# Kernel tuning notes

Hardware: AMD Instinct MI355X
Metric: run time of the kernel (lower is better)

The kernel has to match this reference:

```python
import jax, jax.numpy as jnp
import numpy as np

N_EMB = 256
HEAD_SIZE = 64
B, S = 4, 4096


def setup_inputs() -> dict:
    key = jax.random.key(0)
    k1, k2, k3, k4 = jax.random.split(key, 4)
    return {
        "ini_emb": jax.random.normal(k1, (B, S, N_EMB), dtype=jnp.float32),
        "wk": jax.random.normal(k2, (N_EMB, HEAD_SIZE), dtype=jnp.float32) * (N_EMB ** -0.5),
        "wq": jax.random.normal(k3, (N_EMB, HEAD_SIZE), dtype=jnp.float32) * (N_EMB ** -0.5),
        "wv": jax.random.normal(k4, (N_EMB, HEAD_SIZE), dtype=jnp.float32) * (N_EMB ** -0.5),
    }


def reference(ini_emb, wk, wq, wv):
    # projections: [B,S,E] @ [E,H] -> [B,S,H]
    k = ini_emb @ wk
    q = ini_emb @ wq
    v = ini_emb @ wv
    # scores: [B,S,S]; NOTE: source scales by n_emb**-0.5, not head_size**-0.5
    scores = jnp.einsum("bqh,bkh->bqk", q, k) * (N_EMB ** -0.5)
    attn = jax.nn.softmax(scores, axis=-1)
    # output: [B,S,H]
    return jnp.einsum("bqk,bkh->bqh", attn, v)
```

## Files before the change

kernel.cpp:

```cpp
#include <hip/hip_runtime.h>


typedef short short4v __attribute__((ext_vector_type(4)));
typedef short short8v __attribute__((ext_vector_type(8)));
typedef float floatx4 __attribute__((ext_vector_type(4)));
typedef unsigned short u16;
typedef unsigned int u32;

#define SEQ 4096
#define EMB 256
#define HD 64
#define PADA 264
#define OSTR 68

static __device__ __forceinline__ u16 f2bf(float x) {
    union { float f; unsigned u; } v; v.f = x;
    unsigned r = v.u + 0x7FFFu + ((v.u >> 16) & 1u);
    return (u16)(r >> 16);
}

static __device__ __forceinline__ u32 cvt_pk_bf16(float a, float b) {
    u32 r;
    asm("v_cvt_pk_bf16_f32 %0, %1, %2" : "=v"(r) : "v"(a), "v"(b));
    return r;
}

static __device__ __forceinline__ short4v pack_bf4(float a, float b, float c, float d) {
    union { u32 u[2]; short4v s; } x;
    x.u[0] = cvt_pk_bf16(a, b);
    x.u[1] = cvt_pk_bf16(c, d);
    return x.s;
}

__global__ __launch_bounds__(256) void prep_w(
    const float* __restrict__ wk, const float* __restrict__ wq, const float* __restrict__ wv,
    u16* __restrict__ wt) {
    const int nt = blockIdx.x;
    const int t = threadIdx.x;
#pragma unroll
    for (int ss = 0; ss < 2; ++ss) {
        int slot = t + ss * 256;
        int kc = slot >> 6, lane = slot & 63;
        int ln15 = lane & 15, lq = lane >> 4;
        int cg = nt * 16 + ln15;
        int mat = cg >> 6, col = cg & 63;
        const float* W = (mat == 0) ? wq : (mat == 1) ? wk : wv;
        const float s = (mat == 0) ? 0.0625f * 1.44269504088896f : 1.0f;
        u32 w4[4];
#pragma unroll
        for (int p = 0; p < 2; ++p) {
#pragma unroll
            for (int d = 0; d < 2; ++d) {
                int e0 = kc * 32 + lq * 8 + p * 4 + d * 2;
                u16 lo = f2bf(W[(e0 + 0) * HD + col] * s);
                u16 hi = f2bf(W[(e0 + 1) * HD + col] * s);
                w4[p * 2 + d] = (u32)lo | ((u32)hi << 16);
            }
        }
        u32* dst = (u32*)wt + ((size_t)(nt * 8 + kc) * 64 + lane) * 4;
        *(uint4*)dst = make_uint4(w4[0], w4[1], w4[2], w4[3]);
    }
}

__global__ __launch_bounds__(256) void proj_mfma(
    const float* __restrict__ emb, const u16* __restrict__ wt,
    u16* __restrict__ qb, u16* __restrict__ kb, u16* __restrict__ vbt) {
    __shared__ u16 a_s[16 * PADA];
    const int t = threadIdx.x;
    const int lane = t & 63;
    const int wave = t >> 6;
    const int ln15 = lane & 15;
    const int lq = lane >> 4;
    const size_t row0 = (size_t)blockIdx.x * 16;

#pragma unroll
    for (int c = 0; c < 4; ++c) {
        int f = t + c * 256;
        int row = f >> 6, e4 = (f & 63) * 4;
        float4 v = *(const float4*)(emb + (row0 + row) * EMB + e4);
        u32 lo = cvt_pk_bf16(v.x, v.y);
        u32 hi = cvt_pk_bf16(v.z, v.w);
        *(uint2*)&a_s[row * PADA + e4] = make_uint2(lo, hi);
    }
    __syncthreads();

    floatx4 acc[3];
#pragma unroll
    for (int j = 0; j < 3; ++j) {
        floatx4 z = { 0.f, 0.f, 0.f, 0.f };
        acc[j] = z;
    }

#pragma unroll
    for (int kc = 0; kc < 8; ++kc) {
        short8v a = *(const short8v*)&a_s[ln15 * PADA + kc * 32 + lq * 8];
#pragma unroll
        for (int j = 0; j < 3; ++j) {
            short8v b = *(const short8v*)(wt + (((size_t)(wave * 3 + j) * 8 + kc) * 64 + lane) * 8);
            acc[j] = __builtin_amdgcn_mfma_f32_16x16x32_bf16(a, b, acc[j], 0, 0, 0);
        }
    }

#pragma unroll
    for (int j = 0; j < 3; ++j) {
        int cg = (wave * 3 + j) * 16 + ln15;
        int mat = cg >> 6, col = cg & 63;
        if (mat < 2) {
            u16* O = (mat == 0) ? qb : kb;
#pragma unroll
            for (int r = 0; r < 4; ++r)
                O[(row0 + lq * 4 + r) * HD + col] = f2bf(acc[j][r]);
        } else {
            u32 lo = cvt_pk_bf16(acc[j][0], acc[j][1]);
            u32 hi = cvt_pk_bf16(acc[j][2], acc[j][3]);
            size_t bidx = row0 >> 12;
            size_t sl = (row0 & 4095) + lq * 4;
            *(uint2*)&vbt[(bidx * 64 + col) * SEQ + sl] = make_uint2(lo, hi);
        }
    }
}


__global__ __launch_bounds__(256) void attn_kernel(
    const u16* __restrict__ qb, const u16* __restrict__ kb, const u16* __restrict__ vbt,
    float* __restrict__ po, float* __restrict__ pml) {
    __shared__ __align__(16) u16 smem[4][64 * 64];
    __shared__ float lred[4 * 64];

    const int t = threadIdx.x;
    const int lane = t & 63;
    const int wave = t >> 6;
    const int ln15 = lane & 15;
    const int lq = lane >> 4;

    const int part = ((blockIdx.x & 7) << 6) | (blockIdx.x >> 3);
    const int b = part >> 7;
    const int qt = (part >> 1) & 63;
    const int split = part & 1;
    const int q0 = qt * 64;

    const u16* __restrict__ qpb = qb + ((size_t)b * SEQ + q0) * HD;
    const u16* __restrict__ kpb = kb + (size_t)b * SEQ * HD;
    const u16* __restrict__ vpb = vbt + (size_t)b * HD * SEQ;

    short8v qf[4][2];
#pragma unroll
    for (int nt = 0; nt < 4; ++nt)
#pragma unroll
        for (int h = 0; h < 2; ++h)
            qf[nt][h] = *(const short8v*)(qpb + (size_t)(nt * 16 + ln15) * HD + h * 32 + lq * 8);

    floatx4 oacc[4][4];
#pragma unroll
    for (int ht = 0; ht < 4; ++ht)
#pragma unroll
        for (int nt = 0; nt < 4; ++nt) {
            floatx4 z = { 0.f, 0.f, 0.f, 0.f };
            oacc[ht][nt] = z;
        }
    float lacc[4] = { 0.f, 0.f, 0.f, 0.f };

    const int r0 = t >> 3, c0 = t & 7;
    const int r1 = (t + 256) >> 3, c1 = t & 7;
    const int sw0 = r0 * 64 + ((c0 ^ (r0 & 7)) * 8);
    const int sw1 = r1 * 64 + ((c1 ^ (r1 & 7)) * 8);

    const int krow = wave * 16 + ln15;
    const int ksw_lo = krow * 64 + (((0 + lq) ^ (ln15 & 7)) * 8);
    const int ksw_hi = krow * 64 + (((4 + lq) ^ (ln15 & 7)) * 8);
    const int vch = wave * 2 + (lq >> 1);
    const int voff = ((vch ^ (ln15 & 7)) * 8) + (lq & 1) * 4;

    uint4 ka, kb4, va, vb4;
    {
        const int kwb = (split * 32) * 64;
        ka  = *(const uint4*)(kpb + (size_t)(kwb + r0) * HD + c0 * 8);
        kb4 = *(const uint4*)(kpb + (size_t)(kwb + r1) * HD + c1 * 8);
        va  = *(const uint4*)(vpb + (size_t)r0 * SEQ + kwb + c0 * 8);
        vb4 = *(const uint4*)(vpb + (size_t)r1 * SEQ + kwb + c1 * 8);
        *(uint4*)(&smem[0][0] + sw0) = ka;
        *(uint4*)(&smem[0][0] + sw1) = kb4;
        *(uint4*)(&smem[1][0] + sw0) = va;
        *(uint4*)(&smem[1][0] + sw1) = vb4;
    }
    __syncthreads();

#pragma unroll 1
    for (int tt = 0; tt < 32; ++tt) {
        const int buf = tt & 1;
        if (tt < 31) {
            const int kwb = (split * 32 + tt + 1) * 64;
            ka  = *(const uint4*)(kpb + (size_t)(kwb + r0) * HD + c0 * 8);
            kb4 = *(const uint4*)(kpb + (size_t)(kwb + r1) * HD + c1 * 8);
            va  = *(const uint4*)(vpb + (size_t)r0 * SEQ + kwb + c0 * 8);
            vb4 = *(const uint4*)(vpb + (size_t)r1 * SEQ + kwb + c1 * 8);
        }

        const u16* kt = &smem[buf * 2 + 0][0];
        const u16* vt = &smem[buf * 2 + 1][0];

        short4v vf[4];
#pragma unroll
        for (int ht = 0; ht < 4; ++ht)
            vf[ht] = *(const short4v*)(vt + (ht * 16 + ln15) * 64 + voff);

        short8v k0 = *(const short8v*)(kt + ksw_lo);
        short8v k1 = *(const short8v*)(kt + ksw_hi);

        floatx4 s[4];
        __builtin_amdgcn_s_setprio(1);
#pragma unroll
        for (int nt = 0; nt < 4; ++nt) {
            floatx4 z = { 0.f, 0.f, 0.f, 0.f };
            s[nt] = __builtin_amdgcn_mfma_f32_16x16x32_bf16(k0, qf[nt][0], z, 0, 0, 0);
            s[nt] = __builtin_amdgcn_mfma_f32_16x16x32_bf16(k1, qf[nt][1], s[nt], 0, 0, 0);
        }
        __builtin_amdgcn_s_setprio(0);

        short4v pf[4];
#pragma unroll
        for (int nt = 0; nt < 4; ++nt) {
            float p0 = __builtin_amdgcn_exp2f(s[nt][0]);
            float p1 = __builtin_amdgcn_exp2f(s[nt][1]);
            float p2 = __builtin_amdgcn_exp2f(s[nt][2]);
            float p3 = __builtin_amdgcn_exp2f(s[nt][3]);
            lacc[nt] += (p0 + p1) + (p2 + p3);
            pf[nt] = pack_bf4(p0, p1, p2, p3);
        }

        __builtin_amdgcn_s_setprio(1);
#pragma unroll
        for (int ht = 0; ht < 4; ++ht)
#pragma unroll
            for (int nt = 0; nt < 4; ++nt)
                oacc[ht][nt] = __builtin_amdgcn_mfma_f32_16x16x16bf16_1k(
                    vf[ht], pf[nt], oacc[ht][nt], 0, 0, 0);
        __builtin_amdgcn_s_setprio(0);

        if (tt < 31) {
            u16* ktn = &smem[(buf ^ 1) * 2 + 0][0];
            u16* vtn = &smem[(buf ^ 1) * 2 + 1][0];
            *(uint4*)(ktn + sw0) = ka;
            *(uint4*)(ktn + sw1) = kb4;
            *(uint4*)(vtn + sw0) = va;
            *(uint4*)(vtn + sw1) = vb4;
        }
        __syncthreads();
    }

#pragma unroll
    for (int nt = 0; nt < 4; ++nt) {
        lacc[nt] += __shfl_xor(lacc[nt], 16);
        lacc[nt] += __shfl_xor(lacc[nt], 32);
    }
    if (lq == 0) {
#pragma unroll
        for (int nt = 0; nt < 4; ++nt)
            lred[wave * 64 + nt * 16 + ln15] = lacc[nt];
    }

    float* ored = (float*)&smem[0][0];
    for (int s4 = 0; s4 < 4; ++s4) {
        if (wave == s4) {
#pragma unroll
            for (int nt = 0; nt < 4; ++nt)
#pragma unroll
                for (int ht = 0; ht < 4; ++ht) {
                    int idx = (nt * 16 + ln15) * OSTR + ht * 16 + lq * 4;
                    if (s4 == 0) {
                        *(floatx4*)&ored[idx] = oacc[ht][nt];
                    } else {
                        floatx4 old = *(floatx4*)&ored[idx];
                        old += oacc[ht][nt];
                        *(floatx4*)&ored[idx] = old;
                    }
                }
        }
        __syncthreads();
    }

    float* __restrict__ pob = po + (size_t)part * 4096;
#pragma unroll
    for (int i = 0; i < 4; ++i) {
        int f4 = t + i * 256;
        int q = f4 >> 4, h4 = (f4 & 15) * 4;
        *(float4*)&pob[q * HD + h4] = *(float4*)&ored[q * OSTR + h4];
    }
    if (t < 64)
        pml[part * 64 + t] = lred[t] + lred[64 + t] + lred[128 + t] + lred[192 + t];
}

__global__ __launch_bounds__(256) void reduce_kernel(
    const float* __restrict__ po, const float* __restrict__ pml,
    float* __restrict__ out) {
    __shared__ float ls[64];
    const int t = threadIdx.x;
    const int part0 = blockIdx.x * 2;
    const int bq = blockIdx.x;

    if (t < 64)
        ls[t] = pml[(part0 + 0) * 64 + t] + pml[(part0 + 1) * 64 + t];
    __syncthreads();

    const float* __restrict__ p0 = po + (size_t)(part0 + 0) * 4096;
    const float* __restrict__ p1 = po + (size_t)(part0 + 1) * 4096;
    float* __restrict__ ob = out + (((size_t)(bq >> 6) * SEQ + (size_t)(bq & 63) * 64)) * HD;

#pragma unroll
    for (int i = 0; i < 4; ++i) {
        int f4 = t + i * 256;
        int f = f4 * 4;
        int q = f4 >> 4;
        float4 a = *(const float4*)&p0[f];
        float4 c = *(const float4*)&p1[f];
        float inv = 1.0f / ls[q];
        float4 r;
        r.x = (a.x + c.x) * inv;
        r.y = (a.y + c.y) * inv;
        r.z = (a.z + c.z) * inv;
        r.w = (a.w + c.w) * inv;
        *(float4*)&ob[f] = r;
    }
}

extern "C" void kernel_launch(void* const* d_in, const int* in_sizes, int n_in,
                              void* d_out, int out_size, void* d_ws, size_t ws_size,
                              hipStream_t stream) {
    const float* emb = (const float*)d_in[0];
    const float* wk  = (const float*)d_in[1];
    const float* wq  = (const float*)d_in[2];
    const float* wv  = (const float*)d_in[3];

    u16* qb  = (u16*)d_ws;
    u16* kb  = (u16*)((char*)d_ws + (size_t)2 * 1024 * 1024);
    u16* vbt = (u16*)((char*)d_ws + (size_t)4 * 1024 * 1024);
    u16* wt  = (u16*)((char*)d_ws + (size_t)6 * 1024 * 1024);
    float* po  = (float*)((char*)d_ws + (size_t)6 * 1024 * 1024 + 256 * 1024);
    float* pml = (float*)((char*)d_ws + (size_t)22 * 1024 * 1024 + 256 * 1024);
    float* out = (float*)d_out;

    prep_w<<<12, 256, 0, stream>>>(wk, wq, wv, wt);
    proj_mfma<<<1024, 256, 0, stream>>>(emb, wt, qb, kb, vbt);
    attn_kernel<<<512, 256, 0, stream>>>(qb, kb, vbt, po, pml);
    reduce_kernel<<<256, 256, 0, stream>>>(po, pml, out);
}
```

Baseline: 112.7 us.

## Partition queries across waves with 128-query blocks and four-way KV split

The attention kernel now gives each block 128 queries and a quarter of the keys instead of 64 queries and half the keys. Each wave owns 32 query rows and loops over all 64 keys of the tile, where before each wave took 16 keys for all 64 queries. This removes the cross-wave LDS reduction of the output accumulators and the partial sums, so each wave writes its partials straight to global memory. The cost is more global partial data (four splits of 8192 floats per block), a reduce kernel that sums four partials, and more LDS reads per wave for K and V fragments.

```diff
diff --git a/kernel.cpp b/kernel.cpp
--- a/kernel.cpp
+++ b/kernel.cpp
@@ -11,7 +11,6 @@
 #define EMB 256
 #define HD 64
 #define PADA 264
-#define OSTR 68
 
 static __device__ __forceinline__ u16 f2bf(float x) {
     union { float f; unsigned u; } v; v.f = x;
@@ -125,7 +124,6 @@
     const u16* __restrict__ qb, const u16* __restrict__ kb, const u16* __restrict__ vbt,
     float* __restrict__ po, float* __restrict__ pml) {
     __shared__ __align__(16) u16 smem[4][64 * 64];
-    __shared__ float lred[4 * 64];
 
     const int t = threadIdx.x;
     const int lane = t & 63;
@@ -135,49 +133,47 @@
 
     const int part = ((blockIdx.x & 7) << 6) | (blockIdx.x >> 3);
     const int b = part >> 7;
-    const int qt = (part >> 1) & 63;
-    const int split = part & 1;
-    const int q0 = qt * 64;
+    const int qblk = (part >> 2) & 31;
+    const int split = part & 3;
+    const int q0 = qblk * 128;
 
     const u16* __restrict__ qpb = qb + ((size_t)b * SEQ + q0) * HD;
     const u16* __restrict__ kpb = kb + (size_t)b * SEQ * HD;
     const u16* __restrict__ vpb = vbt + (size_t)b * HD * SEQ;
 
-    short8v qf[4][2];
-#pragma unroll
-    for (int nt = 0; nt < 4; ++nt)
+    short8v qf[2][2];
+#pragma unroll
+    for (int nt = 0; nt < 2; ++nt)
 #pragma unroll
         for (int h = 0; h < 2; ++h)
-            qf[nt][h] = *(const short8v*)(qpb + (size_t)(nt * 16 + ln15) * HD + h * 32 + lq * 8);
-
-    floatx4 oacc[4][4];
+            qf[nt][h] = *(const short8v*)(qpb + (size_t)(wave * 32 + nt * 16 + ln15) * HD + h * 32 + lq * 8);
+
+    floatx4 oacc[4][2];
 #pragma unroll
     for (int ht = 0; ht < 4; ++ht)
 #pragma unroll
-        for (int nt = 0; nt < 4; ++nt) {
+        for (int nt = 0; nt < 2; ++nt) {
             floatx4 z = { 0.f, 0.f, 0.f, 0.f };
             oacc[ht][nt] = z;
         }
-    float lacc[4] = { 0.f, 0.f, 0.f, 0.f };
-
-    const int r0 = t >> 3, c0 = t & 7;
-    const int r1 = (t + 256) >> 3, c1 = t & 7;
+    float lacc[2] = { 0.f, 0.f };
+
+    const int r0 = t >> 3, c0 = t & 7, r1 = r0 + 32;
     const int sw0 = r0 * 64 + ((c0 ^ (r0 & 7)) * 8);
-    const int sw1 = r1 * 64 + ((c1 ^ (r1 & 7)) * 8);
-
-    const int krow = wave * 16 + ln15;
-    const int ksw_lo = krow * 64 + (((0 + lq) ^ (ln15 & 7)) * 8);
-    const int ksw_hi = krow * 64 + (((4 + lq) ^ (ln15 & 7)) * 8);
-    const int vch = wave * 2 + (lq >> 1);
-    const int voff = ((vch ^ (ln15 & 7)) * 8) + (lq & 1) * 4;
+    const int sw1 = r1 * 64 + ((c0 ^ (r1 & 7)) * 8);
+
+    const int xk = ln15 & 7;
+    const int ksw_lo = ln15 * 64 + ((lq ^ xk) * 8);
+    const int ksw_hi = ln15 * 64 + (((4 + lq) ^ xk) * 8);
+    const int vch0 = lq >> 1, vsub = (lq & 1) * 4;
 
     uint4 ka, kb4, va, vb4;
     {
-        const int kwb = (split * 32) * 64;
+        const int kwb = (split * 16) * 64;
         ka  = *(const uint4*)(kpb + (size_t)(kwb + r0) * HD + c0 * 8);
-        kb4 = *(const uint4*)(kpb + (size_t)(kwb + r1) * HD + c1 * 8);
+        kb4 = *(const uint4*)(kpb + (size_t)(kwb + r1) * HD + c0 * 8);
         va  = *(const uint4*)(vpb + (size_t)r0 * SEQ + kwb + c0 * 8);
-        vb4 = *(const uint4*)(vpb + (size_t)r1 * SEQ + kwb + c1 * 8);
+        vb4 = *(const uint4*)(vpb + (size_t)r1 * SEQ + kwb + c0 * 8);
         *(uint4*)(&smem[0][0] + sw0) = ka;
         *(uint4*)(&smem[0][0] + sw1) = kb4;
         *(uint4*)(&smem[1][0] + sw0) = va;
@@ -186,58 +182,59 @@
     __syncthreads();
 
 #pragma unroll 1
-    for (int tt = 0; tt < 32; ++tt) {
+    for (int tt = 0; tt < 16; ++tt) {
         const int buf = tt & 1;
-        if (tt < 31) {
-            const int kwb = (split * 32 + tt + 1) * 64;
+        if (tt < 15) {
+            const int kwb = (split * 16 + tt + 1) * 64;
             ka  = *(const uint4*)(kpb + (size_t)(kwb + r0) * HD + c0 * 8);
-            kb4 = *(const uint4*)(kpb + (size_t)(kwb + r1) * HD + c1 * 8);
+            kb4 = *(const uint4*)(kpb + (size_t)(kwb + r1) * HD + c0 * 8);
             va  = *(const uint4*)(vpb + (size_t)r0 * SEQ + kwb + c0 * 8);
-            vb4 = *(const uint4*)(vpb + (size_t)r1 * SEQ + kwb + c1 * 8);
-        }
-
-        const u16* kt = &smem[buf * 2 + 0][0];
-        const u16* vt = &smem[buf * 2 + 1][0];
-
-        short4v vf[4];
-#pragma unroll
-        for (int ht = 0; ht < 4; ++ht)
-            vf[ht] = *(const short4v*)(vt + (ht * 16 + ln15) * 64 + voff);
-
-        short8v k0 = *(const short8v*)(kt + ksw_lo);
-        short8v k1 = *(const short8v*)(kt + ksw_hi);
-
-        floatx4 s[4];
-        __builtin_amdgcn_s_setprio(1);
-#pragma unroll
-        for (int nt = 0; nt < 4; ++nt) {
-            floatx4 z = { 0.f, 0.f, 0.f, 0.f };
-            s[nt] = __builtin_amdgcn_mfma_f32_16x16x32_bf16(k0, qf[nt][0], z, 0, 0, 0);
-            s[nt] = __builtin_amdgcn_mfma_f32_16x16x32_bf16(k1, qf[nt][1], s[nt], 0, 0, 0);
-        }
-        __builtin_amdgcn_s_setprio(0);
-
-        short4v pf[4];
-#pragma unroll
-        for (int nt = 0; nt < 4; ++nt) {
-            float p0 = __builtin_amdgcn_exp2f(s[nt][0]);
-            float p1 = __builtin_amdgcn_exp2f(s[nt][1]);
-            float p2 = __builtin_amdgcn_exp2f(s[nt][2]);
-            float p3 = __builtin_amdgcn_exp2f(s[nt][3]);
-            lacc[nt] += (p0 + p1) + (p2 + p3);
-            pf[nt] = pack_bf4(p0, p1, p2, p3);
-        }
-
-        __builtin_amdgcn_s_setprio(1);
-#pragma unroll
-        for (int ht = 0; ht < 4; ++ht)
-#pragma unroll
-            for (int nt = 0; nt < 4; ++nt)
-                oacc[ht][nt] = __builtin_amdgcn_mfma_f32_16x16x16bf16_1k(
-                    vf[ht], pf[nt], oacc[ht][nt], 0, 0, 0);
-        __builtin_amdgcn_s_setprio(0);
-
-        if (tt < 31) {
+            vb4 = *(const uint4*)(vpb + (size_t)r1 * SEQ + kwb + c0 * 8);
+        }
+
+        const u16* ktp = &smem[buf * 2 + 0][0];
+        const u16* vtp = &smem[buf * 2 + 1][0];
+
+#pragma unroll
+        for (int kt = 0; kt < 4; ++kt) {
+            short8v k0 = *(const short8v*)(ktp + kt * 1024 + ksw_lo);
+            short8v k1 = *(const short8v*)(ktp + kt * 1024 + ksw_hi);
+
+            floatx4 s[2];
+            __builtin_amdgcn_s_setprio(1);
+#pragma unroll
+            for (int nt = 0; nt < 2; ++nt) {
+                floatx4 z = { 0.f, 0.f, 0.f, 0.f };
+                s[nt] = __builtin_amdgcn_mfma_f32_16x16x32_bf16(k0, qf[nt][0], z, 0, 0, 0);
+                s[nt] = __builtin_amdgcn_mfma_f32_16x16x32_bf16(k1, qf[nt][1], s[nt], 0, 0, 0);
+            }
+            __builtin_amdgcn_s_setprio(0);
+
+            short4v pf[2];
+#pragma unroll
+            for (int nt = 0; nt < 2; ++nt) {
+                float p0 = __builtin_amdgcn_exp2f(s[nt][0]);
+                float p1 = __builtin_amdgcn_exp2f(s[nt][1]);
+                float p2 = __builtin_amdgcn_exp2f(s[nt][2]);
+                float p3 = __builtin_amdgcn_exp2f(s[nt][3]);
+                lacc[nt] += (p0 + p1) + (p2 + p3);
+                pf[nt] = pack_bf4(p0, p1, p2, p3);
+            }
+
+            __builtin_amdgcn_s_setprio(1);
+#pragma unroll
+            for (int ht = 0; ht < 4; ++ht) {
+                short4v vf = *(const short4v*)(vtp + ht * 1024 + ln15 * 64
+                               + (((kt * 2 + vch0) ^ xk) * 8) + vsub);
+#pragma unroll
+                for (int nt = 0; nt < 2; ++nt)
+                    oacc[ht][nt] = __builtin_amdgcn_mfma_f32_16x16x16bf16_1k(
+                        vf, pf[nt], oacc[ht][nt], 0, 0, 0);
+            }
+            __builtin_amdgcn_s_setprio(0);
+        }
+
+        if (tt < 15) {
             u16* ktn = &smem[(buf ^ 1) * 2 + 0][0];
             u16* vtn = &smem[(buf ^ 1) * 2 + 1][0];
             *(uint4*)(ktn + sw0) = ka;
@@ -249,76 +246,59 @@
     }
 
 #pragma unroll
-    for (int nt = 0; nt < 4; ++nt) {
+    for (int nt = 0; nt < 2; ++nt) {
         lacc[nt] += __shfl_xor(lacc[nt], 16);
         lacc[nt] += __shfl_xor(lacc[nt], 32);
     }
     if (lq == 0) {
 #pragma unroll
-        for (int nt = 0; nt < 4; ++nt)
-            lred[wave * 64 + nt * 16 + ln15] = lacc[nt];
-    }
-
-    float* ored = (float*)&smem[0][0];
-    for (int s4 = 0; s4 < 4; ++s4) {
-        if (wave == s4) {
-#pragma unroll
-            for (int nt = 0; nt < 4; ++nt)
-#pragma unroll
-                for (int ht = 0; ht < 4; ++ht) {
-                    int idx = (nt * 16 + ln15) * OSTR + ht * 16 + lq * 4;
-                    if (s4 == 0) {
-                        *(floatx4*)&ored[idx] = oacc[ht][nt];
-                    } else {
-                        floatx4 old = *(floatx4*)&ored[idx];
-                        old += oacc[ht][nt];
-                        *(floatx4*)&ored[idx] = old;
-                    }
-                }
-        }
-        __syncthreads();
-    }
-
-    float* __restrict__ pob = po + (size_t)part * 4096;
-#pragma unroll
-    for (int i = 0; i < 4; ++i) {
-        int f4 = t + i * 256;
-        int q = f4 >> 4, h4 = (f4 & 15) * 4;
-        *(float4*)&pob[q * HD + h4] = *(float4*)&ored[q * OSTR + h4];
-    }
-    if (t < 64)
-        pml[part * 64 + t] = lred[t] + lred[64 + t] + lred[128 + t] + lred[192 + t];
+        for (int nt = 0; nt < 2; ++nt)
+            pml[(size_t)part * 128 + wave * 32 + nt * 16 + ln15] = lacc[nt];
+    }
+
+    float* __restrict__ pob = po + (size_t)part * 8192;
+#pragma unroll
+    for (int ht = 0; ht < 4; ++ht)
+#pragma unroll
+        for (int nt = 0; nt < 2; ++nt)
+            *(floatx4*)&pob[(wave * 32 + nt * 16 + ln15) * 64 + ht * 16 + lq * 4] = oacc[ht][nt];
 }
 
 __global__ __launch_bounds__(256) void reduce_kernel(
     const float* __restrict__ po, const float* __restrict__ pml,
     float* __restrict__ out) {
-    __shared__ float ls[64];
+    __shared__ float ls[128];
     const int t = threadIdx.x;
-    const int part0 = blockIdx.x * 2;
-    const int bq = blockIdx.x;
-
-    if (t < 64)
-        ls[t] = pml[(part0 + 0) * 64 + t] + pml[(part0 + 1) * 64 + t];
+    const int bq = blockIdx.x >> 1;
+    const int half = blockIdx.x & 1;
+    const int part0 = bq * 4;
+
+    if (t < 128)
+        ls[t] = pml[(size_t)(part0 + 0) * 128 + t] + pml[(size_t)(part0 + 1) * 128 + t]
+              + pml[(size_t)(part0 + 2) * 128 + t] + pml[(size_t)(part0 + 3) * 128 + t];
     __syncthreads();
 
-    const float* __restrict__ p0 = po + (size_t)(part0 + 0) * 4096;
-    const float* __restrict__ p1 = po + (size_t)(part0 + 1) * 4096;
-    float* __restrict__ ob = out + (((size_t)(bq >> 6) * SEQ + (size_t)(bq & 63) * 64)) * HD;
+    const float* __restrict__ p0 = po + (size_t)(part0 + 0) * 8192;
+    const float* __restrict__ p1 = po + (size_t)(part0 + 1) * 8192;
+    const float* __restrict__ p2 = po + (size_t)(part0 + 2) * 8192;
+    const float* __restrict__ p3 = po + (size_t)(part0 + 3) * 8192;
+    float* __restrict__ ob = out + ((size_t)(bq >> 5) * SEQ + (size_t)(bq & 31) * 128) * HD;
 
 #pragma unroll
     for (int i = 0; i < 4; ++i) {
-        int f4 = t + i * 256;
+        int f4 = half * 1024 + t + i * 256;
         int f = f4 * 4;
         int q = f4 >> 4;
         float4 a = *(const float4*)&p0[f];
         float4 c = *(const float4*)&p1[f];
+        float4 d = *(const float4*)&p2[f];
+        float4 e = *(const float4*)&p3[f];
         float inv = 1.0f / ls[q];
         float4 r;
-        r.x = (a.x + c.x) * inv;
-        r.y = (a.y + c.y) * inv;
-        r.z = (a.z + c.z) * inv;
-        r.w = (a.w + c.w) * inv;
+        r.x = (a.x + c.x + d.x + e.x) * inv;
+        r.y = (a.y + c.y + d.y + e.y) * inv;
+        r.z = (a.z + c.z + d.z + e.z) * inv;
+        r.w = (a.w + c.w + d.w + e.w) * inv;
         *(float4*)&ob[f] = r;
     }
 }
```

New measurement: 114.7 us. About the same (+1.7%).
